# Kernel tuning notes

Measured on AMD Instinct MI355X. Metric: run time of the kernel, lower is better.

Reference implementation:

```python
import jax, jax.numpy as jnp
import numpy as np

N_LAYER = 2


def setup_inputs() -> dict:
    key = jax.random.key(0)
    k1, k2 = jax.random.split(key)
    seq_len, batch, hidden = 2048, 32, 512
    x = jax.random.normal(k1, (seq_len, batch, hidden), dtype=jnp.float32)
    # torch init: uniform(0, 1) on recurrent weights
    w_hh = jax.random.uniform(k2, (N_LAYER, hidden), dtype=jnp.float32)
    h0 = jnp.zeros((N_LAYER, batch, hidden), dtype=jnp.float32)
    return {"x": x, "w_hh": w_hh, "h0": h0}


def reference(x, w_hh, h0):
    # x: [T, B, H]; w_hh: [L, H]; h0: [L, B, H]
    out = x
    for i in range(N_LAYER):
        w = w_hh[i]  # [H]

        def step(h, xt):
            h_new = jax.nn.relu(xt + h * w)
            return h_new, h_new

        _, out = jax.lax.scan(step, h0[i], out)  # out: [T, B, H]
    return out
```

## Files before the change

kernel.cpp:

```cpp
#include <hip/hip_runtime.h>


#define TSTEPS 2048
#define BATCH  32
#define HID    512
#define BH     (BATCH * HID)
#define U      16
#define D      4
#define NBLK   (TSTEPS / U)

__global__ __launch_bounds__(64, 1) void indrnn_fused_kernel(
    const float* __restrict__ x,
    const float* __restrict__ w_hh,
    const float* __restrict__ h0,
    float* __restrict__ out) {
  const int c   = blockIdx.x * 64 + threadIdx.x;
  const int hid = c & (HID - 1);

  const float w1 = w_hh[hid];
  const float w2 = w_hh[HID + hid];
  float h1 = h0[c];
  float h2 = h0[BH + c];

  const float* xp = x + c;
  float*       op = out + c;

  float buf[D][U];

#pragma unroll
  for (int d = 0; d < D - 1; ++d) {
    const float* xn = xp + (size_t)d * U * BH;
#pragma unroll
    for (int u = 0; u < U; ++u)
      buf[d][u] = xn[(size_t)u * BH];
  }

  for (int blk0 = 0; blk0 < NBLK; blk0 += D) {
#pragma unroll
    for (int d = 0; d < D; ++d) {
      const int blk  = blk0 + d;
      const int pblk = blk + (D - 1);
      if (pblk < NBLK) {
        const float* xn = xp + (size_t)pblk * U * BH;
#pragma unroll
        for (int u = 0; u < U; ++u)
          buf[(d + D - 1) & (D - 1)][u] = xn[(size_t)u * BH];
      }
      float* ob = op + (size_t)blk * U * BH;
#pragma unroll
      for (int u = 0; u < U; ++u) {
        h1 = fmaxf(fmaf(w1, h1, buf[d][u]), 0.0f);
        h2 = fmaxf(fmaf(w2, h2, h1), 0.0f);
        ob[(size_t)u * BH] = h2;
      }
    }
  }
}

extern "C" void kernel_launch(void* const* d_in, const int* in_sizes, int n_in,
                              void* d_out, int out_size, void* d_ws, size_t ws_size,
                              hipStream_t stream) {
  const float* x    = (const float*)d_in[0];
  const float* w_hh = (const float*)d_in[1];
  const float* h0   = (const float*)d_in[2];
  float* out        = (float*)d_out;

  dim3 grid(BH / 64);
  dim3 block(64);
  hipLaunchKernelGGL(indrnn_fused_kernel, grid, block, 0, stream,
                     x, w_hh, h0, out);
}
```

Measured before the change: 241.2 us.

## Split IndRNN kernel into producer wave streaming x into LDS ring and consumer wave

Each block now has two waves. A producer wave issues asynchronous global-to-LDS loads (global_load_lds) into a 4-slot ring of 64-timestep phases, and a consumer wave runs the two-layer recurrence out of LDS and writes the outputs. The two waves hand off slots through barriers and vmcnt waits. This puts much more read traffic in flight and takes the input loads off the recurrence wave's critical path, which was limited by its per-lane register prefetch. The cost is extra barriers, LDS use and more complex hand-off logic.

```diff
diff --git a/kernel.cpp b/kernel.cpp
--- a/kernel.cpp
+++ b/kernel.cpp
@@ -1,59 +1,92 @@
 #include <hip/hip_runtime.h>
 
 
-#define TSTEPS 2048
-#define BATCH  32
-#define HID    512
-#define BH     (BATCH * HID)
-#define U      16
-#define D      4
-#define NBLK   (TSTEPS / U)
+#define TSTEPS  2048
+#define BATCH   32
+#define HID     512
+#define BH      (BATCH * HID)
+#define PHASE_T 64
+#define NPHASE  (TSTEPS / PHASE_T)
+#define NSLOT   4
+#define SLOT_FLOATS (PHASE_T * 64)
+#define SLOT_BYTES  (SLOT_FLOATS * 4)
+#define LOADS_PER_PHASE (PHASE_T / 4)
 
-__global__ __launch_bounds__(64, 1) void indrnn_fused_kernel(
+typedef __attribute__((address_space(1))) const void* gas_cvp;
+typedef __attribute__((address_space(3))) void*       las_vp;
+
+__global__ __launch_bounds__(128, 1) void indrnn_pc_kernel(
     const float* __restrict__ x,
     const float* __restrict__ w_hh,
     const float* __restrict__ h0,
     float* __restrict__ out) {
-  const int c   = blockIdx.x * 64 + threadIdx.x;
-  const int hid = c & (HID - 1);
+  __shared__ float lds[NSLOT * SLOT_FLOATS];
 
-  const float w1 = w_hh[hid];
-  const float w2 = w_hh[HID + hid];
-  float h1 = h0[c];
-  float h2 = h0[BH + c];
+  const int tid   = threadIdx.x;
+  const int wave  = tid >> 6;
+  const int lane  = tid & 63;
+  const int cbase = blockIdx.x * 64;
 
-  const float* xp = x + c;
-  float*       op = out + c;
-
-  float buf[D][U];
+  if (wave == 0) {
+    const int j = lane >> 4;
+    const int i = lane & 15;
+    const float* gp = x + cbase + (size_t)j * BH + i * 4;
 
 #pragma unroll
-  for (int d = 0; d < D - 1; ++d) {
-    const float* xn = xp + (size_t)d * U * BH;
+    for (int p = 0; p < 3; ++p) {
+      char* lbase = (char*)lds + p * SLOT_BYTES;
+      const float* gq = gp + (size_t)p * PHASE_T * BH;
 #pragma unroll
-    for (int u = 0; u < U; ++u)
-      buf[d][u] = xn[(size_t)u * BH];
-  }
+      for (int q = 0; q < LOADS_PER_PHASE; ++q) {
+        __builtin_amdgcn_global_load_lds((gas_cvp)(gq + (size_t)q * 4 * BH),
+                                         (las_vp)(lbase + q * 1024), 16, 0, 0);
+      }
+    }
+    __builtin_amdgcn_sched_barrier(0);
+    asm volatile("s_waitcnt vmcnt(32)" ::: "memory");
+    __builtin_amdgcn_s_barrier();
 
-  for (int blk0 = 0; blk0 < NBLK; blk0 += D) {
+    for (int p = 0; p < NPHASE; ++p) {
+      const int ip = p + 3;
+      if (ip < NPHASE) {
+        char* lbase = (char*)lds + (ip & (NSLOT - 1)) * SLOT_BYTES;
+        const float* gq = gp + (size_t)ip * PHASE_T * BH;
 #pragma unroll
-    for (int d = 0; d < D; ++d) {
-      const int blk  = blk0 + d;
-      const int pblk = blk + (D - 1);
-      if (pblk < NBLK) {
-        const float* xn = xp + (size_t)pblk * U * BH;
+        for (int q = 0; q < LOADS_PER_PHASE; ++q) {
+          __builtin_amdgcn_global_load_lds((gas_cvp)(gq + (size_t)q * 4 * BH),
+                                           (las_vp)(lbase + q * 1024), 16, 0, 0);
+        }
+      }
+      __builtin_amdgcn_sched_barrier(0);
+      if (p < NPHASE - 3)       asm volatile("s_waitcnt vmcnt(32)" ::: "memory");
+      else if (p == NPHASE - 3) asm volatile("s_waitcnt vmcnt(16)" ::: "memory");
+      else                      asm volatile("s_waitcnt vmcnt(0)"  ::: "memory");
+      __builtin_amdgcn_s_barrier();
+    }
+  } else {
+    const int c   = cbase + lane;
+    const int hid = c & (HID - 1);
+    const float w1 = w_hh[hid];
+    const float w2 = w_hh[HID + hid];
+    float h1 = h0[c];
+    float h2 = h0[BH + c];
+    float* op = out + c;
+
+    for (int p = 0; p < NPHASE; ++p) {
+      __builtin_amdgcn_s_barrier();
+      __builtin_amdgcn_sched_barrier(0);
+      const float* lb = lds + (p & (NSLOT - 1)) * SLOT_FLOATS + lane;
+      float* ob = op + (size_t)p * PHASE_T * BH;
 #pragma unroll
-        for (int u = 0; u < U; ++u)
-          buf[(d + D - 1) & (D - 1)][u] = xn[(size_t)u * BH];
-      }
-      float* ob = op + (size_t)blk * U * BH;
-#pragma unroll
-      for (int u = 0; u < U; ++u) {
-        h1 = fmaxf(fmaf(w1, h1, buf[d][u]), 0.0f);
+      for (int u = 0; u < PHASE_T; ++u) {
+        const float xv = lb[u * 64];
+        h1 = fmaxf(fmaf(w1, h1, xv), 0.0f);
         h2 = fmaxf(fmaf(w2, h2, h1), 0.0f);
         ob[(size_t)u * BH] = h2;
       }
+      __builtin_amdgcn_sched_barrier(0);
     }
+    __builtin_amdgcn_s_barrier();
   }
 }
 
@@ -66,7 +99,7 @@
   float* out        = (float*)d_out;
 
   dim3 grid(BH / 64);
-  dim3 block(64);
-  hipLaunchKernelGGL(indrnn_fused_kernel, grid, block, 0, stream,
+  dim3 block(128);
+  hipLaunchKernelGGL(indrnn_pc_kernel, grid, block, 0, stream,
                      x, w_hh, h0, out);
 }
```

New measurement: 231.0 us. 4.2% less time.

## Split each wave across timestep quads and broadcast inputs via lane shuffles

Applied to the files above, without the earlier changes.

Each 64-lane wave now covers 16 hidden columns instead of 64. The four lane groups each load a different timestep of a 4-step quad, and every lane pulls all four inputs for its column with __shfl. Each lane runs the serial recurrence redundantly and keeps only the output for its own timestep, so loads and stores are spread across lanes. The grid grows fourfold, giving more waves per CU to hide memory latency. The cost is redundant compute, shuffle instructions, and narrower 64-byte contiguous segments per memory row.

```diff
diff --git a/kernel.cpp b/kernel.cpp
--- a/kernel.cpp
+++ b/kernel.cpp
@@ -5,54 +5,55 @@
 #define BATCH  32
 #define HID    512
 #define BH     (BATCH * HID)
-#define U      16
-#define D      4
-#define NBLK   (TSTEPS / U)
+#define CPB    16
+#define QT     4
+#define NQ     (TSTEPS / QT)
+#define P      16
 
-__global__ __launch_bounds__(64, 1) void indrnn_fused_kernel(
+__global__ __launch_bounds__(64, 1) void indrnn_tq_kernel(
     const float* __restrict__ x,
     const float* __restrict__ w_hh,
     const float* __restrict__ h0,
     float* __restrict__ out) {
-  const int c   = blockIdx.x * 64 + threadIdx.x;
-  const int hid = c & (HID - 1);
+  const int lane  = threadIdx.x;
+  const int i     = lane & 15;
+  const int j     = lane >> 4;
+  const int cbase = blockIdx.x * CPB;
+  const int c     = cbase + i;
+  const int hid   = c & (HID - 1);
 
   const float w1 = w_hh[hid];
   const float w2 = w_hh[HID + hid];
   float h1 = h0[c];
   float h2 = h0[BH + c];
 
-  const float* xp = x + c;
-  float*       op = out + c;
+  const size_t goff = (size_t)j * BH + c;
+  const float* xp = x + goff;
+  float*       op = out + goff;
 
-  float buf[D][U];
+  float buf[P];
+#pragma unroll
+  for (int q = 0; q < P; ++q)
+    buf[q] = xp[(size_t)q * QT * BH];
 
+  for (int qq = 0; qq < NQ; qq += P) {
 #pragma unroll
-  for (int d = 0; d < D - 1; ++d) {
-    const float* xn = xp + (size_t)d * U * BH;
+    for (int d = 0; d < P; ++d) {
+      const int q  = qq + d;
+      const float xv = buf[d];
+      const int pq = q + P;
+      if (pq < NQ)
+        buf[d] = xp[(size_t)pq * QT * BH];
+
+      float sval = 0.0f;
 #pragma unroll
-    for (int u = 0; u < U; ++u)
-      buf[d][u] = xn[(size_t)u * BH];
-  }
-
-  for (int blk0 = 0; blk0 < NBLK; blk0 += D) {
-#pragma unroll
-    for (int d = 0; d < D; ++d) {
-      const int blk  = blk0 + d;
-      const int pblk = blk + (D - 1);
-      if (pblk < NBLK) {
-        const float* xn = xp + (size_t)pblk * U * BH;
-#pragma unroll
-        for (int u = 0; u < U; ++u)
-          buf[(d + D - 1) & (D - 1)][u] = xn[(size_t)u * BH];
+      for (int u = 0; u < QT; ++u) {
+        const float xu = __shfl(xv, u * 16 + i, 64);
+        h1 = fmaxf(fmaf(w1, h1, xu), 0.0f);
+        h2 = fmaxf(fmaf(w2, h2, h1), 0.0f);
+        if (u == j) sval = h2;
       }
-      float* ob = op + (size_t)blk * U * BH;
-#pragma unroll
-      for (int u = 0; u < U; ++u) {
-        h1 = fmaxf(fmaf(w1, h1, buf[d][u]), 0.0f);
-        h2 = fmaxf(fmaf(w2, h2, h1), 0.0f);
-        ob[(size_t)u * BH] = h2;
-      }
+      op[(size_t)q * QT * BH] = sval;
     }
   }
 }
@@ -65,8 +66,8 @@
   const float* h0   = (const float*)d_in[2];
   float* out        = (float*)d_out;
 
-  dim3 grid(BH / 64);
+  dim3 grid(BH / CPB);
   dim3 block(64);
-  hipLaunchKernelGGL(indrnn_fused_kernel, grid, block, 0, stream,
+  hipLaunchKernelGGL(indrnn_tq_kernel, grid, block, 0, stream,
                      x, w_hh, h0, out);
 }
```

New measurement: 484.2 us. 101% more time.
